# Kernel tuning notes

Hardware: AMD Instinct MI355X
Metric: run time of the kernel (lower is better)

## Reference

```python
import jax, jax.numpy as jnp
import numpy as np

HEADS = 10
DIM_HEAD = 64
C = 640
N_TOK = 1024          # (1024//32)**2 tokens per image
IMG_NUMS = 3          # total_length = id_length + 1
ID_LENGTH = 2
SA = 0.5
NEG_INF = -1e9


def _build_story_mask(key):
    # Faithful to cal_attn_mask_xl: one random row of columns shared by all
    # images, columns beyond the id_length reference images zeroed, and each
    # image's own block forced True; then broadcast over query tokens.
    L = IMG_NUMS * N_TOK
    base = jax.random.uniform(key, (1, L)) < SA                  # [1, L]
    bm = jnp.tile(base, (IMG_NUMS, 1))                           # [img, L]
    col = jnp.arange(L)
    bm = jnp.where(col[None, :] >= ID_LENGTH * N_TOK, False, bm)
    self_block = (col // N_TOK)[None, :] == jnp.arange(IMG_NUMS)[:, None]
    bm = bm | self_block                                         # [img, L]
    return jnp.repeat(bm, N_TOK, axis=0)                         # [L, L]


def setup_inputs() -> dict:
    key = jax.random.key(0)
    ks = jax.random.split(key, 7)
    B_total = 2 * IMG_NUMS
    hidden_states = jax.random.normal(ks[0], (B_total, N_TOK, C), dtype=jnp.float32)
    mask = _build_story_mask(ks[1])
    s = 1.0 / np.sqrt(C)
    Wq = jax.random.normal(ks[2], (C, HEADS * DIM_HEAD), dtype=jnp.float32) * s
    Wk = jax.random.normal(ks[3], (C, HEADS * DIM_HEAD), dtype=jnp.float32) * s
    Wv = jax.random.normal(ks[4], (C, HEADS * DIM_HEAD), dtype=jnp.float32) * s
    Wout = jax.random.normal(ks[5], (HEADS * DIM_HEAD, C), dtype=jnp.float32) * s
    bout = jnp.zeros((C,), dtype=jnp.float32)
    return {"hidden_states": hidden_states, "mask": mask,
            "Wq": Wq, "Wk": Wk, "Wv": Wv, "Wout": Wout, "bout": bout}


def reference(hidden_states, mask, Wq, Wk, Wv, Wout, bout):
    # __call1__ with encoder_hidden_states=None: fuse img_nums images into one
    # long sequence per CFG branch, then masked SDPA.
    B_total, n_tok, c = hidden_states.shape
    img_nums = B_total // 2
    L = img_nums * n_tok
    x = hidden_states.reshape(2, L, c)                       # [2, L, C]

    q = jnp.einsum('bsc,cd->bsd', x, Wq).reshape(2, L, HEADS, DIM_HEAD)
    k = jnp.einsum('bsc,cd->bsd', x, Wk).reshape(2, L, HEADS, DIM_HEAD)
    v = jnp.einsum('bsc,cd->bsd', x, Wv).reshape(2, L, HEADS, DIM_HEAD)

    scale = 1.0 / jnp.sqrt(jnp.asarray(DIM_HEAD, dtype=q.dtype))
    scores = jnp.einsum('bqhd,bkhd->bhqk', q, k) * scale     # [2, H, L, L]
    scores = jnp.where(mask[None, None, :, :], scores, NEG_INF)
    attn = jax.nn.softmax(scores, axis=-1)
    out = jnp.einsum('bhqk,bkhd->bqhd', attn, v)             # [2, L, H, Dh]
    out = out.reshape(B_total, n_tok, HEADS * DIM_HEAD)
    return jnp.einsum('bsd,dc->bsc', out, Wout) + bout
```

## Files before the change

kernel.cpp:

```cpp
#include <hip/hip_runtime.h>
#include <cstdint>
#include <cstddef>

typedef _Float16 f16;
typedef _Float16 f16x8 __attribute__((ext_vector_type(8)));
typedef _Float16 f16x4 __attribute__((ext_vector_type(4)));
typedef float f32x4 __attribute__((ext_vector_type(4)));

#define MFMA32(a, b, c) __builtin_amdgcn_mfma_f32_16x16x32_f16((a), (b), (c), 0, 0, 0)
#define MFMA16(a, b, c) __builtin_amdgcn_mfma_f32_16x16x16f16((a), (b), (c), 0, 0, 0)

#if __has_builtin(__builtin_amdgcn_exp2f)
#define EXP2F(x) __builtin_amdgcn_exp2f(x)
#else
#define EXP2F(x) exp2f(x)
#endif

#define DRAIN_MEM() __builtin_amdgcn_s_waitcnt(0x0070)

#define LOG2E 1.44269504088896340736f

__device__ __forceinline__ f16x4 pack4(float a, float b, float c, float d) {
    f16x4 r; r[0] = (f16)a; r[1] = (f16)b; r[2] = (f16)c; r[3] = (f16)d;
    return r;
}

__device__ __forceinline__ void gl_lds16(const f16* g, f16* l) {
    __builtin_amdgcn_global_load_lds((const __attribute__((address_space(1))) void*)g,
                                     (__attribute__((address_space(3))) void*)l, 16, 0, 0);
}

__global__ __launch_bounds__(256) void k_cvt_x(const float4* __restrict__ x, f16x4* __restrict__ xb) {
    const int i = blockIdx.x * 256 + threadIdx.x;
    const float4 v = x[i];
    f16x4 o;
    o[0] = (f16)v.x; o[1] = (f16)v.y; o[2] = (f16)v.z; o[3] = (f16)v.w;
    xb[i] = o;
}

__global__ __launch_bounds__(256) void k_cvt_w(const float* __restrict__ Wq, const float* __restrict__ Wk,
                                               const float* __restrict__ Wv, const float* __restrict__ Wo,
                                               f16* __restrict__ WT, f16* __restrict__ WoT) {
    __shared__ float tile[32][33];
    const int z = blockIdx.z;
    const float* src = (z == 0) ? Wq : (z == 1) ? Wk : (z == 2) ? Wv : Wo;
    f16* dst = (z < 3) ? (WT + (size_t)z * 640 * 640) : WoT;
    const float scale = (z == 0) ? 0.125f * LOG2E : 1.0f;
    const int k0 = blockIdx.x * 32, n0 = blockIdx.y * 32;
    const int t = threadIdx.x;
#pragma unroll
    for (int i = 0; i < 4; i++) {
        const int idx = i * 256 + t;
        const int r = idx >> 5, c = idx & 31;
        tile[r][c] = src[(size_t)(k0 + r) * 640 + n0 + c];
    }
    __syncthreads();
#pragma unroll
    for (int i = 0; i < 4; i++) {
        const int idx = i * 256 + t;
        const int r = idx >> 5, c = idx & 31;
        dst[(size_t)(n0 + r) * 640 + k0 + c] = (f16)(tile[c][r] * scale);
    }
}

__global__ __launch_bounds__(256) void k_gemm(const f16* __restrict__ A, const f16* __restrict__ B,
                                              f16* __restrict__ qb, f16* __restrict__ kb, f16* __restrict__ vtb) {
    __shared__ f16 As[128 * 40];
    __shared__ f16 Bs[128 * 40];
    const int t = threadIdx.x;
    const int wave = t >> 6, lane = t & 63, quad = lane >> 4, l16 = lane & 15;
    const int wm = wave >> 1, wn = wave & 1;
    const long m0 = (long)blockIdx.x * 128, n0 = (long)blockIdx.y * 128;
    const int srow = t >> 2, skc = t & 3;

    const f32x4 zero = {0.f, 0.f, 0.f, 0.f};
    f32x4 acc[4][4];
#pragma unroll
    for (int i = 0; i < 4; i++)
#pragma unroll
        for (int j = 0; j < 4; j++) acc[i][j] = zero;

    const f16* gA1 = A + (m0 + srow) * 640 + skc * 8;
    const f16* gA2 = A + (m0 + 64 + srow) * 640 + skc * 8;
    const f16* gB1 = B + (n0 + srow) * 640 + skc * 8;
    const f16* gB2 = B + (n0 + 64 + srow) * 640 + skc * 8;
    f16* sA1 = As + srow * 40 + skc * 8;
    f16* sA2 = As + (64 + srow) * 40 + skc * 8;
    f16* sB1 = Bs + srow * 40 + skc * 8;
    f16* sB2 = Bs + (64 + srow) * 40 + skc * 8;

    for (int kt = 0; kt < 20; kt++) {
        const int ko = kt * 32;
        const f16x8 a1 = *(const f16x8*)(gA1 + ko);
        const f16x8 a2 = *(const f16x8*)(gA2 + ko);
        const f16x8 b1 = *(const f16x8*)(gB1 + ko);
        const f16x8 b2 = *(const f16x8*)(gB2 + ko);
        __syncthreads();
        *(f16x8*)sA1 = a1;
        *(f16x8*)sA2 = a2;
        *(f16x8*)sB1 = b1;
        *(f16x8*)sB2 = b2;
        __syncthreads();
        f16x8 af[4], bfr[4];
#pragma unroll
        for (int mi = 0; mi < 4; mi++) af[mi] = *(const f16x8*)(As + (wm * 64 + mi * 16 + l16) * 40 + quad * 8);
#pragma unroll
        for (int ni = 0; ni < 4; ni++) bfr[ni] = *(const f16x8*)(Bs + (wn * 64 + ni * 16 + l16) * 40 + quad * 8);
#pragma unroll
        for (int mi = 0; mi < 4; mi++)
#pragma unroll
            for (int ni = 0; ni < 4; ni++) acc[mi][ni] = MFMA32(af[mi], bfr[ni], acc[mi][ni]);
    }

    const int b = (int)(m0 / 3072);
    const int which = (int)(n0 / 640);
    const int hd0 = (int)(n0 - (long)which * 640);
    if (which < 2) {
        f16* dst = (which == 0) ? qb : kb;
#pragma unroll
        for (int ni = 0; ni < 4; ni++) {
            const int hd = hd0 + wn * 64 + ni * 16 + l16;
            const int h = hd >> 6, d = hd & 63;
#pragma unroll
            for (int mi = 0; mi < 4; mi++) {
                const long l0 = m0 - (long)b * 3072 + wm * 64 + mi * 16 + quad * 4;
                f16* p = dst + ((long)(b * 10 + h) * 3072 + l0) * 64 + d;
#pragma unroll
                for (int j = 0; j < 4; j++) p[(long)j * 64] = (f16)acc[mi][ni][j];
            }
        }
    } else {
#pragma unroll
        for (int ni = 0; ni < 4; ni++) {
            const int hd = hd0 + wn * 64 + ni * 16 + l16;
            const int h = hd >> 6, d = hd & 63;
#pragma unroll
            for (int mi = 0; mi < 4; mi++) {
                const long l0 = m0 - (long)b * 3072 + wm * 64 + mi * 16 + quad * 4;
                const long col = (l0 & ~63L) + quad * 16 + mi * 4;
                f16x4 tmp;
#pragma unroll
                for (int j = 0; j < 4; j++) tmp[j] = (f16)acc[mi][ni][j];
                *(f16x4*)(vtb + ((size_t)(b * 10 + h) * 64 + d) * 3072 + col) = tmp;
            }
        }
    }
}

__global__ __launch_bounds__(256) void k_gemmo(const f16* __restrict__ A, const f16* __restrict__ B,
                                               float* __restrict__ out, const float* __restrict__ bias) {
    __shared__ f16 As[64 * 40];
    __shared__ f16 Bs[128 * 40];
    const int t = threadIdx.x;
    const int wave = t >> 6, lane = t & 63, quad = lane >> 4, l16 = lane & 15;
    const int wm = wave >> 1, wn = wave & 1;
    const long m0 = (long)blockIdx.x * 64, n0 = (long)blockIdx.y * 128;
    const int srow = t >> 2, skc = t & 3;

    const f32x4 zero = {0.f, 0.f, 0.f, 0.f};
    f32x4 acc[2][4];
#pragma unroll
    for (int i = 0; i < 2; i++)
#pragma unroll
        for (int j = 0; j < 4; j++) acc[i][j] = zero;

    const f16* gA = A + (m0 + srow) * 640 + skc * 8;
    const f16* gB1 = B + (n0 + srow) * 640 + skc * 8;
    const f16* gB2 = B + (n0 + 64 + srow) * 640 + skc * 8;
    f16* sA = As + srow * 40 + skc * 8;
    f16* sB1 = Bs + srow * 40 + skc * 8;
    f16* sB2 = Bs + (64 + srow) * 40 + skc * 8;

    for (int kt = 0; kt < 20; kt++) {
        const int ko = kt * 32;
        const f16x8 a1 = *(const f16x8*)(gA + ko);
        const f16x8 b1 = *(const f16x8*)(gB1 + ko);
        const f16x8 b2 = *(const f16x8*)(gB2 + ko);
        __syncthreads();
        *(f16x8*)sA = a1;
        *(f16x8*)sB1 = b1;
        *(f16x8*)sB2 = b2;
        __syncthreads();
        f16x8 af[2], bfr[4];
#pragma unroll
        for (int mi = 0; mi < 2; mi++) af[mi] = *(const f16x8*)(As + (wm * 32 + mi * 16 + l16) * 40 + quad * 8);
#pragma unroll
        for (int ni = 0; ni < 4; ni++) bfr[ni] = *(const f16x8*)(Bs + (wn * 64 + ni * 16 + l16) * 40 + quad * 8);
#pragma unroll
        for (int mi = 0; mi < 2; mi++)
#pragma unroll
            for (int ni = 0; ni < 4; ni++) acc[mi][ni] = MFMA32(af[mi], bfr[ni], acc[mi][ni]);
    }

#pragma unroll
    for (int ni = 0; ni < 4; ni++) {
        const long gc = n0 + wn * 64 + ni * 16 + l16;
        const float bs = bias[gc];
#pragma unroll
        for (int mi = 0; mi < 2; mi++) {
            const long r0 = m0 + wm * 32 + mi * 16 + quad * 4;
            float* p = out + r0 * 640 + gc;
#pragma unroll
            for (int j = 0; j < 4; j++) p[(long)j * 640] = acc[mi][ni][j] + bs;
        }
    }
}

__global__ __launch_bounds__(128, 2) void k_attn(const f16* __restrict__ q, const f16* __restrict__ k,
                                                 const f16* __restrict__ vT, const unsigned char* __restrict__ mask,
                                                 f16* __restrict__ ao) {
    __shared__ __align__(16) unsigned char smem[40960];

    const int t = threadIdx.x;
    const int w = t >> 6, lane = t & 63, quad = lane >> 4, l16 = lane & 15;
    const int bh = blockIdx.y, b = bh / 10, h = bh - b * 10;
    const int qt = (blockIdx.x < 16) ? (32 + (int)blockIdx.x) : ((int)blockIdx.x - 16);
    const int q0 = qt * 64;
    const int img = q0 >> 10;
    const int kmax = (img == 2) ? 3072 : 2048;
    const int nIter = kmax >> 6;
    float* bias_s = (float*)(smem + 32768);

    int mmode;
    if (mask[1] && mask[2] && mask[3]) mmode = 0;
    else if (mask[7] == 0x3f) mmode = 2;
    else mmode = 1;
    const int msz = (mmode == 0) ? 1 : 4;
    const int mhi = (mmode == 2) ? 3 : 0;
    const unsigned char* mrow = mask + (size_t)img * 1024 * 3072 * msz;

    for (int i = t; i < 2048; i += 128)
        bias_s[i] = (mrow[(size_t)i * msz + mhi] != 0) ? -8.f : -1e9f;

    const int r8 = lane >> 3, cch = lane & 7;
    const f16* kg = k + (size_t)bh * 3072 * 64;
    const f16* vg = vT + (size_t)bh * 64 * 3072;
    const int wrow0 = w * 32;

    {
        f16* K0 = (f16*)smem;
        f16* V0 = (f16*)(smem + 16384);
#pragma unroll
        for (int i = 0; i < 4; i++) {
            const int row = wrow0 + i * 8 + r8;
            gl_lds16(kg + (size_t)row * 64 + ((cch ^ (row & 7)) * 8), K0 + (wrow0 + i * 8) * 64);
            gl_lds16(vg + (size_t)row * 3072 + ((cch ^ (row & 7)) * 8), V0 + (wrow0 + i * 8) * 64);
        }
    }

    f16x8 qfA0, qfA1, qfB0, qfB1;
    {
        const f16* qp = q + ((size_t)bh * 3072 + q0 + w * 32 + l16) * 64 + quad * 8;
        qfA0 = *(const f16x8*)qp;
        qfA1 = *(const f16x8*)(qp + 32);
        qfB0 = *(const f16x8*)(qp + 16 * 64);
        qfB1 = *(const f16x8*)(qp + 16 * 64 + 32);
    }

    const int s7 = l16 & 7;
    const int bK0 = l16 * 128 + ((quad ^ s7) * 16);
    const int bK1 = l16 * 128 + (((quad + 4) ^ s7) * 16);
    const int bV0 = l16 * 128 + (((2 * quad) ^ s7) * 16);
    const int bV1 = l16 * 128 + (((2 * quad + 1) ^ s7) * 16);

    const f32x4 zero = {0.f, 0.f, 0.f, 0.f};
    f32x4 OA[4], OB[4];
#pragma unroll
    for (int i = 0; i < 4; i++) { OA[i] = zero; OB[i] = zero; }
    float lA = 0.f, lB = 0.f;

    const f32x4 m8 = {-8.f, -8.f, -8.f, -8.f};

    for (int it = 0; it < nIter; it++) {
        DRAIN_MEM();
        __syncthreads();
        const char* Kb = (const char*)smem + (it & 1) * 8192;
        const char* Vb = (const char*)smem + 16384 + (it & 1) * 8192;
        if (it + 1 < nIter) {
            const int k0n = (it + 1) << 6;
            f16* Kn = (f16*)(smem + ((it + 1) & 1) * 8192);
            f16* Vn = (f16*)(smem + 16384 + ((it + 1) & 1) * 8192);
#pragma unroll
            for (int i = 0; i < 4; i++) {
                const int row = wrow0 + i * 8 + r8;
                gl_lds16(kg + (size_t)(k0n + row) * 64 + ((cch ^ (row & 7)) * 8), Kn + (wrow0 + i * 8) * 64);
                gl_lds16(vg + (size_t)row * 3072 + k0n + ((cch ^ (row & 7)) * 8), Vn + (wrow0 + i * 8) * 64);
            }
        }

        f32x4 sA[4], sB[4];
#pragma unroll
        for (int kt = 0; kt < 4; kt++) {
            const f16x8 kf0 = *(const f16x8*)(Kb + bK0 + kt * 2048);
            const f16x8 kf1 = *(const f16x8*)(Kb + bK1 + kt * 2048);
            sA[kt] = MFMA32(kf0, qfA0, zero);
            sA[kt] = MFMA32(kf1, qfA1, sA[kt]);
            sB[kt] = MFMA32(kf0, qfB0, zero);
            sB[kt] = MFMA32(kf1, qfB1, sB[kt]);
        }
        if (it * 64 < 2048) {
#pragma unroll
            for (int kt = 0; kt < 4; kt++) {
                const f32x4 bv = *(const f32x4*)(bias_s + it * 64 + kt * 16 + quad * 4);
                sA[kt] += bv;
                sB[kt] += bv;
            }
        } else {
#pragma unroll
            for (int kt = 0; kt < 4; kt++) { sA[kt] += m8; sB[kt] += m8; }
        }

        f16x4 pkA[4], pkB[4];
#pragma unroll
        for (int kt = 0; kt < 4; kt++) {
            const float a0 = EXP2F(sA[kt][0]), a1 = EXP2F(sA[kt][1]);
            const float a2 = EXP2F(sA[kt][2]), a3 = EXP2F(sA[kt][3]);
            lA += (a0 + a1) + (a2 + a3);
            pkA[kt] = pack4(a0, a1, a2, a3);
            const float b0 = EXP2F(sB[kt][0]), b1 = EXP2F(sB[kt][1]);
            const float b2 = EXP2F(sB[kt][2]), b3 = EXP2F(sB[kt][3]);
            lB += (b0 + b1) + (b2 + b3);
            pkB[kt] = pack4(b0, b1, b2, b3);
        }

#pragma unroll
        for (int mtd = 0; mtd < 4; mtd++) {
            const f16x8 v80 = *(const f16x8*)(Vb + bV0 + mtd * 2048);
            const f16x8 v81 = *(const f16x8*)(Vb + bV1 + mtd * 2048);
            const f16x4 vf0 = __builtin_shufflevector(v80, v80, 0, 1, 2, 3);
            const f16x4 vf1 = __builtin_shufflevector(v80, v80, 4, 5, 6, 7);
            const f16x4 vf2 = __builtin_shufflevector(v81, v81, 0, 1, 2, 3);
            const f16x4 vf3 = __builtin_shufflevector(v81, v81, 4, 5, 6, 7);
            OA[mtd] = MFMA16(vf0, pkA[0], OA[mtd]);
            OA[mtd] = MFMA16(vf1, pkA[1], OA[mtd]);
            OA[mtd] = MFMA16(vf2, pkA[2], OA[mtd]);
            OA[mtd] = MFMA16(vf3, pkA[3], OA[mtd]);
            OB[mtd] = MFMA16(vf0, pkB[0], OB[mtd]);
            OB[mtd] = MFMA16(vf1, pkB[1], OB[mtd]);
            OB[mtd] = MFMA16(vf2, pkB[2], OB[mtd]);
            OB[mtd] = MFMA16(vf3, pkB[3], OB[mtd]);
        }
    }

    lA += __shfl_xor(lA, 16);
    lA += __shfl_xor(lA, 32);
    lB += __shfl_xor(lB, 16);
    lB += __shfl_xor(lB, 32);
    const float invA = 1.0f / lA;
    const float invB = 1.0f / lB;
    f16* orowA = ao + ((size_t)(b * 3072 + q0 + w * 32 + l16)) * 640 + h * 64;
    f16* orowB = orowA + (size_t)16 * 640;
#pragma unroll
    for (int mtd = 0; mtd < 4; mtd++) {
        f16x4 oa, ob;
#pragma unroll
        for (int j = 0; j < 4; j++) { oa[j] = (f16)(OA[mtd][j] * invA); ob[j] = (f16)(OB[mtd][j] * invB); }
        *(f16x4*)(orowA + mtd * 16 + quad * 4) = oa;
        *(f16x4*)(orowB + mtd * 16 + quad * 4) = ob;
    }
}

extern "C" void kernel_launch(void* const* d_in, const int* in_sizes, int n_in,
                              void* d_out, int out_size, void* d_ws, size_t ws_size,
                              hipStream_t stream) {
    (void)in_sizes; (void)n_in; (void)out_size; (void)ws_size;
    const float* x = (const float*)d_in[0];
    const unsigned char* mask = (const unsigned char*)d_in[1];
    const float* Wq = (const float*)d_in[2];
    const float* Wk = (const float*)d_in[3];
    const float* Wv = (const float*)d_in[4];
    const float* Wo = (const float*)d_in[5];
    const float* bout = (const float*)d_in[6];
    float* out = (float*)d_out;

    f16* xb  = (f16*)d_ws;
    f16* WT  = xb + 6144 * 640;
    f16* WoT = WT + 1920 * 640;
    f16* qb  = WoT + 640 * 640;
    f16* kb  = qb + 20 * 3072 * 64;
    f16* vtb = kb + 20 * 3072 * 64;

    k_cvt_x<<<3840, 256, 0, stream>>>((const float4*)x, (f16x4*)xb);
    k_cvt_w<<<dim3(20, 20, 4), 256, 0, stream>>>(Wq, Wk, Wv, Wo, WT, WoT);
    k_gemm<<<dim3(48, 15), 256, 0, stream>>>(xb, WT, qb, kb, vtb);
    k_attn<<<dim3(48, 20), 128, 0, stream>>>(qb, kb, vtb, mask, xb );
    k_gemmo<<<dim3(96, 5), 256, 0, stream>>>(xb, WoT, out, bout);
}
```

Before: 207.8 us.

## Split attention over key range with merge kernel; fuse x conversion into QKV GEMM

The attention kernel now splits each query tile's key range into two halves handled by separate blocks. Each block writes unnormalized fp32 partial outputs and row sums, and a new merge kernel adds the two halves, normalizes them and converts to fp16. This is meant to double the block count and reduce tail imbalance between images with different key lengths. The standalone fp32-to-fp16 conversion of x is removed: the QKV GEMM now reads fp32 directly and converts while loading. In exchange, the split adds fp32 partial-output traffic and one more kernel launch.

```diff
diff --git a/kernel.cpp b/kernel.cpp
--- a/kernel.cpp
+++ b/kernel.cpp
@@ -25,17 +25,16 @@
     return r;
 }
 
+__device__ __forceinline__ f16x8 cvt8(const float4 lo, const float4 hi) {
+    f16x8 r;
+    r[0] = (f16)lo.x; r[1] = (f16)lo.y; r[2] = (f16)lo.z; r[3] = (f16)lo.w;
+    r[4] = (f16)hi.x; r[5] = (f16)hi.y; r[6] = (f16)hi.z; r[7] = (f16)hi.w;
+    return r;
+}
+
 __device__ __forceinline__ void gl_lds16(const f16* g, f16* l) {
     __builtin_amdgcn_global_load_lds((const __attribute__((address_space(1))) void*)g,
                                      (__attribute__((address_space(3))) void*)l, 16, 0, 0);
-}
-
-__global__ __launch_bounds__(256) void k_cvt_x(const float4* __restrict__ x, f16x4* __restrict__ xb) {
-    const int i = blockIdx.x * 256 + threadIdx.x;
-    const float4 v = x[i];
-    f16x4 o;
-    o[0] = (f16)v.x; o[1] = (f16)v.y; o[2] = (f16)v.z; o[3] = (f16)v.w;
-    xb[i] = o;
 }
 
 __global__ __launch_bounds__(256) void k_cvt_w(const float* __restrict__ Wq, const float* __restrict__ Wk,
@@ -63,7 +62,7 @@
     }
 }
 
-__global__ __launch_bounds__(256) void k_gemm(const f16* __restrict__ A, const f16* __restrict__ B,
+__global__ __launch_bounds__(256) void k_gemm(const float* __restrict__ X, const f16* __restrict__ B,
                                               f16* __restrict__ qb, f16* __restrict__ kb, f16* __restrict__ vtb) {
     __shared__ f16 As[128 * 40];
     __shared__ f16 Bs[128 * 40];
@@ -80,8 +79,8 @@
 #pragma unroll
         for (int j = 0; j < 4; j++) acc[i][j] = zero;
 
-    const f16* gA1 = A + (m0 + srow) * 640 + skc * 8;
-    const f16* gA2 = A + (m0 + 64 + srow) * 640 + skc * 8;
+    const float* gA1 = X + (m0 + srow) * 640 + skc * 8;
+    const float* gA2 = X + (m0 + 64 + srow) * 640 + skc * 8;
     const f16* gB1 = B + (n0 + srow) * 640 + skc * 8;
     const f16* gB2 = B + (n0 + 64 + srow) * 640 + skc * 8;
     f16* sA1 = As + srow * 40 + skc * 8;
@@ -91,8 +90,8 @@
 
     for (int kt = 0; kt < 20; kt++) {
         const int ko = kt * 32;
-        const f16x8 a1 = *(const f16x8*)(gA1 + ko);
-        const f16x8 a2 = *(const f16x8*)(gA2 + ko);
+        const f16x8 a1 = cvt8(*(const float4*)(gA1 + ko), *(const float4*)(gA1 + ko + 4));
+        const f16x8 a2 = cvt8(*(const float4*)(gA2 + ko), *(const float4*)(gA2 + ko + 4));
         const f16x8 b1 = *(const f16x8*)(gB1 + ko);
         const f16x8 b2 = *(const f16x8*)(gB2 + ko);
         __syncthreads();
@@ -206,19 +205,38 @@
     }
 }
 
+__global__ __launch_bounds__(256) void k_merge(const float* __restrict__ Op, const float* __restrict__ lp,
+                                               f16* __restrict__ ao) {
+    const int i = (blockIdx.x * 256 + threadIdx.x) * 4;
+    const int qrow = i / 640;
+    const int hd = i - qrow * 640;
+    const int h = hd >> 6;
+    const float l = lp[qrow * 10 + h] + lp[61440 + qrow * 10 + h];
+    const float inv = 1.0f / l;
+    const f32x4 o0 = *(const f32x4*)(Op + i);
+    const f32x4 o1 = *(const f32x4*)(Op + (size_t)6144 * 640 + i);
+    f16x4 o;
+#pragma unroll
+    for (int j = 0; j < 4; j++) o[j] = (f16)((o0[j] + o1[j]) * inv);
+    *(f16x4*)(ao + i) = o;
+}
+
 __global__ __launch_bounds__(128, 2) void k_attn(const f16* __restrict__ q, const f16* __restrict__ k,
                                                  const f16* __restrict__ vT, const unsigned char* __restrict__ mask,
-                                                 f16* __restrict__ ao) {
+                                                 float* __restrict__ Op, float* __restrict__ lp) {
     __shared__ __align__(16) unsigned char smem[40960];
 
     const int t = threadIdx.x;
     const int w = t >> 6, lane = t & 63, quad = lane >> 4, l16 = lane & 15;
     const int bh = blockIdx.y, b = bh / 10, h = bh - b * 10;
-    const int qt = (blockIdx.x < 16) ? (32 + (int)blockIdx.x) : ((int)blockIdx.x - 16);
+    const int split = (int)blockIdx.x & 1;
+    const int qi = (int)blockIdx.x >> 1;
+    const int qt = (qi < 16) ? (32 + qi) : (qi - 16);
     const int q0 = qt * 64;
     const int img = q0 >> 10;
     const int kmax = (img == 2) ? 3072 : 2048;
-    const int nIter = kmax >> 6;
+    const int kbase = split * (kmax >> 1);
+    const int nIter = kmax >> 7;
     float* bias_s = (float*)(smem + 32768);
 
     int mmode;
@@ -243,8 +261,8 @@
 #pragma unroll
         for (int i = 0; i < 4; i++) {
             const int row = wrow0 + i * 8 + r8;
-            gl_lds16(kg + (size_t)row * 64 + ((cch ^ (row & 7)) * 8), K0 + (wrow0 + i * 8) * 64);
-            gl_lds16(vg + (size_t)row * 3072 + ((cch ^ (row & 7)) * 8), V0 + (wrow0 + i * 8) * 64);
+            gl_lds16(kg + (size_t)(kbase + row) * 64 + ((cch ^ (row & 7)) * 8), K0 + (wrow0 + i * 8) * 64);
+            gl_lds16(vg + (size_t)row * 3072 + kbase + ((cch ^ (row & 7)) * 8), V0 + (wrow0 + i * 8) * 64);
         }
     }
 
@@ -276,8 +294,9 @@
         __syncthreads();
         const char* Kb = (const char*)smem + (it & 1) * 8192;
         const char* Vb = (const char*)smem + 16384 + (it & 1) * 8192;
+        const int tb = kbase + it * 64;
         if (it + 1 < nIter) {
-            const int k0n = (it + 1) << 6;
+            const int k0n = tb + 64;
             f16* Kn = (f16*)(smem + ((it + 1) & 1) * 8192);
             f16* Vn = (f16*)(smem + 16384 + ((it + 1) & 1) * 8192);
 #pragma unroll
@@ -298,10 +317,10 @@
             sB[kt] = MFMA32(kf0, qfB0, zero);
             sB[kt] = MFMA32(kf1, qfB1, sB[kt]);
         }
-        if (it * 64 < 2048) {
+        if (tb < 2048) {
 #pragma unroll
             for (int kt = 0; kt < 4; kt++) {
-                const f32x4 bv = *(const f32x4*)(bias_s + it * 64 + kt * 16 + quad * 4);
+                const f32x4 bv = *(const f32x4*)(bias_s + tb + kt * 16 + quad * 4);
                 sA[kt] += bv;
                 sB[kt] += bv;
             }
@@ -346,17 +365,19 @@
     lA += __shfl_xor(lA, 32);
     lB += __shfl_xor(lB, 16);
     lB += __shfl_xor(lB, 32);
-    const float invA = 1.0f / lA;
-    const float invB = 1.0f / lB;
-    f16* orowA = ao + ((size_t)(b * 3072 + q0 + w * 32 + l16)) * 640 + h * 64;
-    f16* orowB = orowA + (size_t)16 * 640;
+    float* Ob = Op + (size_t)split * 6144 * 640;
+    float* lb = lp + (size_t)split * 61440;
+    const int qA = b * 3072 + q0 + w * 32 + l16;
+    if (quad == 0) {
+        lb[(size_t)qA * 10 + h] = lA;
+        lb[(size_t)(qA + 16) * 10 + h] = lB;
+    }
+    float* orowA = Ob + (size_t)qA * 640 + h * 64;
+    float* orowB = orowA + (size_t)16 * 640;
 #pragma unroll
     for (int mtd = 0; mtd < 4; mtd++) {
-        f16x4 oa, ob;
-#pragma unroll
-        for (int j = 0; j < 4; j++) { oa[j] = (f16)(OA[mtd][j] * invA); ob[j] = (f16)(OB[mtd][j] * invB); }
-        *(f16x4*)(orowA + mtd * 16 + quad * 4) = oa;
-        *(f16x4*)(orowB + mtd * 16 + quad * 4) = ob;
+        *(f32x4*)(orowA + mtd * 16 + quad * 4) = OA[mtd];
+        *(f32x4*)(orowB + mtd * 16 + quad * 4) = OB[mtd];
     }
 }
 
@@ -373,16 +394,18 @@
     const float* bout = (const float*)d_in[6];
     float* out = (float*)d_out;
 
-    f16* xb  = (f16*)d_ws;
-    f16* WT  = xb + 6144 * 640;
+    f16* WT  = (f16*)d_ws;
     f16* WoT = WT + 1920 * 640;
     f16* qb  = WoT + 640 * 640;
     f16* kb  = qb + 20 * 3072 * 64;
     f16* vtb = kb + 20 * 3072 * 64;
-
-    k_cvt_x<<<3840, 256, 0, stream>>>((const float4*)x, (f16x4*)xb);
+    f16* ao  = vtb + 20 * 3072 * 64;
+    float* Op = (float*)(ao + 6144 * 640);
+    float* lp = Op + (size_t)2 * 6144 * 640;
+
     k_cvt_w<<<dim3(20, 20, 4), 256, 0, stream>>>(Wq, Wk, Wv, Wo, WT, WoT);
-    k_gemm<<<dim3(48, 15), 256, 0, stream>>>(xb, WT, qb, kb, vtb);
-    k_attn<<<dim3(48, 20), 128, 0, stream>>>(qb, kb, vtb, mask, xb );
-    k_gemmo<<<dim3(96, 5), 256, 0, stream>>>(xb, WoT, out, bout);
-}
+    k_gemm<<<dim3(48, 15), 256, 0, stream>>>(x, WT, qb, kb, vtb);
+    k_attn<<<dim3(96, 20), 128, 0, stream>>>(qb, kb, vtb, mask, Op, lp);
+    k_merge<<<3840, 256, 0, stream>>>(Op, lp, ao);
+    k_gemmo<<<dim3(96, 5), 256, 0, stream>>>(ao, WoT, out, bout);
+}
```

After: 217.0 us. 4.4% more time.

## Fuse x conversion into QKV GEMM, precompute mask bias, single-wave attention blocks

Applied to the files above, without the earlier changes.

Drops the separate fp32-to-fp16 conversion kernel for x, so the QKV GEMM now reads fp32 activations and converts them while staging into LDS. The mask-to-bias table is built once by a small kernel into global memory, replacing the per-block LDS fill in the attention kernel. Attention blocks shrink from two waves to one, each loading full K/V tiles itself and waiting only on its own vmcnt instead of a block barrier, with twice as many blocks. In exchange the GEMM reads twice the A bytes, the bias is now read from global memory every iteration, and each wave issues twice as many async loads.

```diff
diff --git a/kernel.cpp b/kernel.cpp
--- a/kernel.cpp
+++ b/kernel.cpp
@@ -16,7 +16,7 @@
 #define EXP2F(x) exp2f(x)
 #endif
 
-#define DRAIN_MEM() __builtin_amdgcn_s_waitcnt(0x0070)
+#define WAIT_VM0() __builtin_amdgcn_s_waitcnt(0x0F70)
 
 #define LOG2E 1.44269504088896340736f
 
@@ -25,17 +25,30 @@
     return r;
 }
 
+__device__ __forceinline__ f16x8 cvt8(const float4 lo, const float4 hi) {
+    f16x8 r;
+    r[0] = (f16)lo.x; r[1] = (f16)lo.y; r[2] = (f16)lo.z; r[3] = (f16)lo.w;
+    r[4] = (f16)hi.x; r[5] = (f16)hi.y; r[6] = (f16)hi.z; r[7] = (f16)hi.w;
+    return r;
+}
+
 __device__ __forceinline__ void gl_lds16(const f16* g, f16* l) {
     __builtin_amdgcn_global_load_lds((const __attribute__((address_space(1))) void*)g,
                                      (__attribute__((address_space(3))) void*)l, 16, 0, 0);
 }
 
-__global__ __launch_bounds__(256) void k_cvt_x(const float4* __restrict__ x, f16x4* __restrict__ xb) {
+__global__ __launch_bounds__(256) void k_bias(const unsigned char* __restrict__ mask,
+                                              float* __restrict__ bias_g) {
+    int mmode;
+    if (mask[1] && mask[2] && mask[3]) mmode = 0;
+    else if (mask[7] == 0x3f) mmode = 2;
+    else mmode = 1;
+    const int msz = (mmode == 0) ? 1 : 4;
+    const int mhi = (mmode == 2) ? 3 : 0;
     const int i = blockIdx.x * 256 + threadIdx.x;
-    const float4 v = x[i];
-    f16x4 o;
-    o[0] = (f16)v.x; o[1] = (f16)v.y; o[2] = (f16)v.z; o[3] = (f16)v.w;
-    xb[i] = o;
+    const int img = i / 3072, c = i - img * 3072;
+    const unsigned char* mrow = mask + (size_t)img * 1024 * 3072 * msz;
+    bias_g[i] = (mrow[(size_t)c * msz + mhi] != 0) ? -8.f : -1e9f;
 }
 
 __global__ __launch_bounds__(256) void k_cvt_w(const float* __restrict__ Wq, const float* __restrict__ Wk,
@@ -63,7 +76,7 @@
     }
 }
 
-__global__ __launch_bounds__(256) void k_gemm(const f16* __restrict__ A, const f16* __restrict__ B,
+__global__ __launch_bounds__(256) void k_gemm(const float* __restrict__ X, const f16* __restrict__ B,
                                               f16* __restrict__ qb, f16* __restrict__ kb, f16* __restrict__ vtb) {
     __shared__ f16 As[128 * 40];
     __shared__ f16 Bs[128 * 40];
@@ -80,8 +93,8 @@
 #pragma unroll
         for (int j = 0; j < 4; j++) acc[i][j] = zero;
 
-    const f16* gA1 = A + (m0 + srow) * 640 + skc * 8;
-    const f16* gA2 = A + (m0 + 64 + srow) * 640 + skc * 8;
+    const float* gA1 = X + (m0 + srow) * 640 + skc * 8;
+    const float* gA2 = X + (m0 + 64 + srow) * 640 + skc * 8;
     const f16* gB1 = B + (n0 + srow) * 640 + skc * 8;
     const f16* gB2 = B + (n0 + 64 + srow) * 640 + skc * 8;
     f16* sA1 = As + srow * 40 + skc * 8;
@@ -91,8 +104,8 @@
 
     for (int kt = 0; kt < 20; kt++) {
         const int ko = kt * 32;
-        const f16x8 a1 = *(const f16x8*)(gA1 + ko);
-        const f16x8 a2 = *(const f16x8*)(gA2 + ko);
+        const f16x8 a1 = cvt8(*(const float4*)(gA1 + ko), *(const float4*)(gA1 + ko + 4));
+        const f16x8 a2 = cvt8(*(const float4*)(gA2 + ko), *(const float4*)(gA2 + ko + 4));
         const f16x8 b1 = *(const f16x8*)(gB1 + ko);
         const f16x8 b2 = *(const f16x8*)(gB2 + ko);
         __syncthreads();
@@ -206,51 +219,39 @@
     }
 }
 
-__global__ __launch_bounds__(128, 2) void k_attn(const f16* __restrict__ q, const f16* __restrict__ k,
-                                                 const f16* __restrict__ vT, const unsigned char* __restrict__ mask,
-                                                 f16* __restrict__ ao) {
-    __shared__ __align__(16) unsigned char smem[40960];
-
-    const int t = threadIdx.x;
-    const int w = t >> 6, lane = t & 63, quad = lane >> 4, l16 = lane & 15;
+__global__ __launch_bounds__(64, 2) void k_attn(const f16* __restrict__ q, const f16* __restrict__ k,
+                                                const f16* __restrict__ vT, const float* __restrict__ bias_g,
+                                                f16* __restrict__ ao) {
+    __shared__ __align__(16) unsigned char smem[32768];
+
+    const int lane = threadIdx.x;
+    const int quad = lane >> 4, l16 = lane & 15;
     const int bh = blockIdx.y, b = bh / 10, h = bh - b * 10;
-    const int qt = (blockIdx.x < 16) ? (32 + (int)blockIdx.x) : ((int)blockIdx.x - 16);
-    const int q0 = qt * 64;
+    const int wt = (blockIdx.x < 32) ? (64 + (int)blockIdx.x) : ((int)blockIdx.x - 32);
+    const int q0 = wt * 32;
     const int img = q0 >> 10;
     const int kmax = (img == 2) ? 3072 : 2048;
     const int nIter = kmax >> 6;
-    float* bias_s = (float*)(smem + 32768);
-
-    int mmode;
-    if (mask[1] && mask[2] && mask[3]) mmode = 0;
-    else if (mask[7] == 0x3f) mmode = 2;
-    else mmode = 1;
-    const int msz = (mmode == 0) ? 1 : 4;
-    const int mhi = (mmode == 2) ? 3 : 0;
-    const unsigned char* mrow = mask + (size_t)img * 1024 * 3072 * msz;
-
-    for (int i = t; i < 2048; i += 128)
-        bias_s[i] = (mrow[(size_t)i * msz + mhi] != 0) ? -8.f : -1e9f;
+    const float* bg = bias_g + img * 3072;
 
     const int r8 = lane >> 3, cch = lane & 7;
     const f16* kg = k + (size_t)bh * 3072 * 64;
     const f16* vg = vT + (size_t)bh * 64 * 3072;
-    const int wrow0 = w * 32;
 
     {
         f16* K0 = (f16*)smem;
         f16* V0 = (f16*)(smem + 16384);
 #pragma unroll
-        for (int i = 0; i < 4; i++) {
-            const int row = wrow0 + i * 8 + r8;
-            gl_lds16(kg + (size_t)row * 64 + ((cch ^ (row & 7)) * 8), K0 + (wrow0 + i * 8) * 64);
-            gl_lds16(vg + (size_t)row * 3072 + ((cch ^ (row & 7)) * 8), V0 + (wrow0 + i * 8) * 64);
+        for (int i = 0; i < 8; i++) {
+            const int row = i * 8 + r8;
+            gl_lds16(kg + (size_t)row * 64 + ((cch ^ (row & 7)) * 8), K0 + i * 8 * 64);
+            gl_lds16(vg + (size_t)row * 3072 + ((cch ^ (row & 7)) * 8), V0 + i * 8 * 64);
         }
     }
 
     f16x8 qfA0, qfA1, qfB0, qfB1;
     {
-        const f16* qp = q + ((size_t)bh * 3072 + q0 + w * 32 + l16) * 64 + quad * 8;
+        const f16* qp = q + ((size_t)bh * 3072 + q0 + l16) * 64 + quad * 8;
         qfA0 = *(const f16x8*)qp;
         qfA1 = *(const f16x8*)(qp + 32);
         qfB0 = *(const f16x8*)(qp + 16 * 64);
@@ -269,24 +270,26 @@
     for (int i = 0; i < 4; i++) { OA[i] = zero; OB[i] = zero; }
     float lA = 0.f, lB = 0.f;
 
-    const f32x4 m8 = {-8.f, -8.f, -8.f, -8.f};
-
     for (int it = 0; it < nIter; it++) {
-        DRAIN_MEM();
-        __syncthreads();
+        WAIT_VM0();
         const char* Kb = (const char*)smem + (it & 1) * 8192;
         const char* Vb = (const char*)smem + 16384 + (it & 1) * 8192;
+        const int tb = it * 64;
         if (it + 1 < nIter) {
-            const int k0n = (it + 1) << 6;
+            const int k0n = tb + 64;
             f16* Kn = (f16*)(smem + ((it + 1) & 1) * 8192);
             f16* Vn = (f16*)(smem + 16384 + ((it + 1) & 1) * 8192);
 #pragma unroll
-            for (int i = 0; i < 4; i++) {
-                const int row = wrow0 + i * 8 + r8;
-                gl_lds16(kg + (size_t)(k0n + row) * 64 + ((cch ^ (row & 7)) * 8), Kn + (wrow0 + i * 8) * 64);
-                gl_lds16(vg + (size_t)row * 3072 + k0n + ((cch ^ (row & 7)) * 8), Vn + (wrow0 + i * 8) * 64);
+            for (int i = 0; i < 8; i++) {
+                const int row = i * 8 + r8;
+                gl_lds16(kg + (size_t)(k0n + row) * 64 + ((cch ^ (row & 7)) * 8), Kn + i * 8 * 64);
+                gl_lds16(vg + (size_t)row * 3072 + k0n + ((cch ^ (row & 7)) * 8), Vn + i * 8 * 64);
             }
         }
+
+        f32x4 bv[4];
+#pragma unroll
+        for (int kt = 0; kt < 4; kt++) bv[kt] = *(const f32x4*)(bg + tb + kt * 16 + quad * 4);
 
         f32x4 sA[4], sB[4];
 #pragma unroll
@@ -298,17 +301,8 @@
             sB[kt] = MFMA32(kf0, qfB0, zero);
             sB[kt] = MFMA32(kf1, qfB1, sB[kt]);
         }
-        if (it * 64 < 2048) {
-#pragma unroll
-            for (int kt = 0; kt < 4; kt++) {
-                const f32x4 bv = *(const f32x4*)(bias_s + it * 64 + kt * 16 + quad * 4);
-                sA[kt] += bv;
-                sB[kt] += bv;
-            }
-        } else {
-#pragma unroll
-            for (int kt = 0; kt < 4; kt++) { sA[kt] += m8; sB[kt] += m8; }
-        }
+#pragma unroll
+        for (int kt = 0; kt < 4; kt++) { sA[kt] += bv[kt]; sB[kt] += bv[kt]; }
 
         f16x4 pkA[4], pkB[4];
 #pragma unroll
@@ -348,7 +342,7 @@
     lB += __shfl_xor(lB, 32);
     const float invA = 1.0f / lA;
     const float invB = 1.0f / lB;
-    f16* orowA = ao + ((size_t)(b * 3072 + q0 + w * 32 + l16)) * 640 + h * 64;
+    f16* orowA = ao + ((size_t)(b * 3072 + q0 + l16)) * 640 + h * 64;
     f16* orowB = orowA + (size_t)16 * 640;
 #pragma unroll
     for (int mtd = 0; mtd < 4; mtd++) {
@@ -373,16 +367,17 @@
     const float* bout = (const float*)d_in[6];
     float* out = (float*)d_out;
 
-    f16* xb  = (f16*)d_ws;
-    f16* WT  = xb + 6144 * 640;
+    f16* WT  = (f16*)d_ws;
     f16* WoT = WT + 1920 * 640;
     f16* qb  = WoT + 640 * 640;
     f16* kb  = qb + 20 * 3072 * 64;
     f16* vtb = kb + 20 * 3072 * 64;
-
-    k_cvt_x<<<3840, 256, 0, stream>>>((const float4*)x, (f16x4*)xb);
+    f16* ao  = vtb + 20 * 3072 * 64;
+    float* bias_g = (float*)(ao + 6144 * 640);
+
     k_cvt_w<<<dim3(20, 20, 4), 256, 0, stream>>>(Wq, Wk, Wv, Wo, WT, WoT);
-    k_gemm<<<dim3(48, 15), 256, 0, stream>>>(xb, WT, qb, kb, vtb);
-    k_attn<<<dim3(48, 20), 128, 0, stream>>>(qb, kb, vtb, mask, xb );
-    k_gemmo<<<dim3(96, 5), 256, 0, stream>>>(xb, WoT, out, bout);
-}
+    k_bias<<<36, 256, 0, stream>>>(mask, bias_g);
+    k_gemm<<<dim3(48, 15), 256, 0, stream>>>(x, WT, qb, kb, vtb);
+    k_attn<<<dim3(96, 20), 64, 0, stream>>>(qb, kb, vtb, bias_g, ao);
+    k_gemmo<<<dim3(96, 5), 256, 0, stream>>>(ao, WoT, out, bout);
+}
```

New measurement: 275.4 us. +32.5%, slower.

## Double attention query tile per block and merge conversion kernels into one launch

Applied to the files above, without the earlier changes.

The attention kernel now gives each wave 64 query rows (four 16-row chunks) instead of 32, so each K/V tile staged in LDS is reused across twice as many queries and the grid shrinks from 48 to 24 blocks per head. Score computation, bias add, exp and packing are fused into one loop per key subtile. The x and weight conversion kernels are merged into a single launch, and the attention output goes to a separate workspace buffer rather than overwriting xb. In exchange, register pressure rises sharply (16 output accumulators per wave) and there are fewer blocks for 256 CUs, which may hurt occupancy and load balance.

```diff
diff --git a/kernel.cpp b/kernel.cpp
--- a/kernel.cpp
+++ b/kernel.cpp
@@ -30,24 +30,28 @@
                                      (__attribute__((address_space(3))) void*)l, 16, 0, 0);
 }
 
-__global__ __launch_bounds__(256) void k_cvt_x(const float4* __restrict__ x, f16x4* __restrict__ xb) {
-    const int i = blockIdx.x * 256 + threadIdx.x;
-    const float4 v = x[i];
-    f16x4 o;
-    o[0] = (f16)v.x; o[1] = (f16)v.y; o[2] = (f16)v.z; o[3] = (f16)v.w;
-    xb[i] = o;
-}
-
-__global__ __launch_bounds__(256) void k_cvt_w(const float* __restrict__ Wq, const float* __restrict__ Wk,
-                                               const float* __restrict__ Wv, const float* __restrict__ Wo,
-                                               f16* __restrict__ WT, f16* __restrict__ WoT) {
+__global__ __launch_bounds__(256) void k_prep(const float4* __restrict__ x4, f16x4* __restrict__ xb,
+                                              const float* __restrict__ Wq, const float* __restrict__ Wk,
+                                              const float* __restrict__ Wv, const float* __restrict__ Wo,
+                                              f16* __restrict__ WT, f16* __restrict__ WoT) {
     __shared__ float tile[32][33];
-    const int z = blockIdx.z;
+    const int t = threadIdx.x;
+    if (blockIdx.x < 3840) {
+        const int i = blockIdx.x * 256 + t;
+        const float4 v = x4[i];
+        f16x4 o;
+        o[0] = (f16)v.x; o[1] = (f16)v.y; o[2] = (f16)v.z; o[3] = (f16)v.w;
+        xb[i] = o;
+        return;
+    }
+    const int bi = blockIdx.x - 3840;
+    const int z = bi / 400;
+    const int rem = bi - z * 400;
+    const int bx = rem / 20, by = rem - (rem / 20) * 20;
     const float* src = (z == 0) ? Wq : (z == 1) ? Wk : (z == 2) ? Wv : Wo;
     f16* dst = (z < 3) ? (WT + (size_t)z * 640 * 640) : WoT;
     const float scale = (z == 0) ? 0.125f * LOG2E : 1.0f;
-    const int k0 = blockIdx.x * 32, n0 = blockIdx.y * 32;
-    const int t = threadIdx.x;
+    const int k0 = bx * 32, n0 = by * 32;
 #pragma unroll
     for (int i = 0; i < 4; i++) {
         const int idx = i * 256 + t;
@@ -214,8 +218,8 @@
     const int t = threadIdx.x;
     const int w = t >> 6, lane = t & 63, quad = lane >> 4, l16 = lane & 15;
     const int bh = blockIdx.y, b = bh / 10, h = bh - b * 10;
-    const int qt = (blockIdx.x < 16) ? (32 + (int)blockIdx.x) : ((int)blockIdx.x - 16);
-    const int q0 = qt * 64;
+    const int qt = (blockIdx.x < 8) ? (16 + (int)blockIdx.x) : ((int)blockIdx.x - 8);
+    const int q0 = qt * 128;
     const int img = q0 >> 10;
     const int kmax = (img == 2) ? 3072 : 2048;
     const int nIter = kmax >> 6;
@@ -248,13 +252,12 @@
         }
     }
 
-    f16x8 qfA0, qfA1, qfB0, qfB1;
-    {
-        const f16* qp = q + ((size_t)bh * 3072 + q0 + w * 32 + l16) * 64 + quad * 8;
-        qfA0 = *(const f16x8*)qp;
-        qfA1 = *(const f16x8*)(qp + 32);
-        qfB0 = *(const f16x8*)(qp + 16 * 64);
-        qfB1 = *(const f16x8*)(qp + 16 * 64 + 32);
+    f16x8 qf[4][2];
+#pragma unroll
+    for (int c = 0; c < 4; c++) {
+        const f16* qp = q + ((size_t)bh * 3072 + q0 + w * 64 + c * 16 + l16) * 64 + quad * 8;
+        qf[c][0] = *(const f16x8*)qp;
+        qf[c][1] = *(const f16x8*)(qp + 32);
     }
 
     const int s7 = l16 & 7;
@@ -264,10 +267,12 @@
     const int bV1 = l16 * 128 + (((2 * quad + 1) ^ s7) * 16);
 
     const f32x4 zero = {0.f, 0.f, 0.f, 0.f};
-    f32x4 OA[4], OB[4];
-#pragma unroll
-    for (int i = 0; i < 4; i++) { OA[i] = zero; OB[i] = zero; }
-    float lA = 0.f, lB = 0.f;
+    f32x4 O[4][4];
+#pragma unroll
+    for (int c = 0; c < 4; c++)
+#pragma unroll
+        for (int m = 0; m < 4; m++) O[c][m] = zero;
+    float l_i[4] = {0.f, 0.f, 0.f, 0.f};
 
     const f32x4 m8 = {-8.f, -8.f, -8.f, -8.f};
 
@@ -276,8 +281,9 @@
         __syncthreads();
         const char* Kb = (const char*)smem + (it & 1) * 8192;
         const char* Vb = (const char*)smem + 16384 + (it & 1) * 8192;
+        const int tb = it * 64;
         if (it + 1 < nIter) {
-            const int k0n = (it + 1) << 6;
+            const int k0n = tb + 64;
             f16* Kn = (f16*)(smem + ((it + 1) & 1) * 8192);
             f16* Vn = (f16*)(smem + 16384 + ((it + 1) & 1) * 8192);
 #pragma unroll
@@ -288,39 +294,23 @@
             }
         }
 
-        f32x4 sA[4], sB[4];
+        f16x4 pk[4][4];
 #pragma unroll
         for (int kt = 0; kt < 4; kt++) {
             const f16x8 kf0 = *(const f16x8*)(Kb + bK0 + kt * 2048);
             const f16x8 kf1 = *(const f16x8*)(Kb + bK1 + kt * 2048);
-            sA[kt] = MFMA32(kf0, qfA0, zero);
-            sA[kt] = MFMA32(kf1, qfA1, sA[kt]);
-            sB[kt] = MFMA32(kf0, qfB0, zero);
-            sB[kt] = MFMA32(kf1, qfB1, sB[kt]);
-        }
-        if (it * 64 < 2048) {
-#pragma unroll
-            for (int kt = 0; kt < 4; kt++) {
-                const f32x4 bv = *(const f32x4*)(bias_s + it * 64 + kt * 16 + quad * 4);
-                sA[kt] += bv;
-                sB[kt] += bv;
-            }
-        } else {
-#pragma unroll
-            for (int kt = 0; kt < 4; kt++) { sA[kt] += m8; sB[kt] += m8; }
-        }
-
-        f16x4 pkA[4], pkB[4];
-#pragma unroll
-        for (int kt = 0; kt < 4; kt++) {
-            const float a0 = EXP2F(sA[kt][0]), a1 = EXP2F(sA[kt][1]);
-            const float a2 = EXP2F(sA[kt][2]), a3 = EXP2F(sA[kt][3]);
-            lA += (a0 + a1) + (a2 + a3);
-            pkA[kt] = pack4(a0, a1, a2, a3);
-            const float b0 = EXP2F(sB[kt][0]), b1 = EXP2F(sB[kt][1]);
-            const float b2 = EXP2F(sB[kt][2]), b3 = EXP2F(sB[kt][3]);
-            lB += (b0 + b1) + (b2 + b3);
-            pkB[kt] = pack4(b0, b1, b2, b3);
+            f32x4 bv = m8;
+            if (tb < 2048) bv = *(const f32x4*)(bias_s + tb + kt * 16 + quad * 4);
+#pragma unroll
+            for (int c = 0; c < 4; c++) {
+                f32x4 s = MFMA32(kf0, qf[c][0], zero);
+                s = MFMA32(kf1, qf[c][1], s);
+                s += bv;
+                const float p0 = EXP2F(s[0]), p1 = EXP2F(s[1]);
+                const float p2 = EXP2F(s[2]), p3 = EXP2F(s[3]);
+                l_i[c] += (p0 + p1) + (p2 + p3);
+                pk[c][kt] = pack4(p0, p1, p2, p3);
+            }
         }
 
 #pragma unroll
@@ -331,32 +321,29 @@
             const f16x4 vf1 = __builtin_shufflevector(v80, v80, 4, 5, 6, 7);
             const f16x4 vf2 = __builtin_shufflevector(v81, v81, 0, 1, 2, 3);
             const f16x4 vf3 = __builtin_shufflevector(v81, v81, 4, 5, 6, 7);
-            OA[mtd] = MFMA16(vf0, pkA[0], OA[mtd]);
-            OA[mtd] = MFMA16(vf1, pkA[1], OA[mtd]);
-            OA[mtd] = MFMA16(vf2, pkA[2], OA[mtd]);
-            OA[mtd] = MFMA16(vf3, pkA[3], OA[mtd]);
-            OB[mtd] = MFMA16(vf0, pkB[0], OB[mtd]);
-            OB[mtd] = MFMA16(vf1, pkB[1], OB[mtd]);
-            OB[mtd] = MFMA16(vf2, pkB[2], OB[mtd]);
-            OB[mtd] = MFMA16(vf3, pkB[3], OB[mtd]);
-        }
-    }
-
-    lA += __shfl_xor(lA, 16);
-    lA += __shfl_xor(lA, 32);
-    lB += __shfl_xor(lB, 16);
-    lB += __shfl_xor(lB, 32);
-    const float invA = 1.0f / lA;
-    const float invB = 1.0f / lB;
-    f16* orowA = ao + ((size_t)(b * 3072 + q0 + w * 32 + l16)) * 640 + h * 64;
-    f16* orowB = orowA + (size_t)16 * 640;
-#pragma unroll
-    for (int mtd = 0; mtd < 4; mtd++) {
-        f16x4 oa, ob;
-#pragma unroll
-        for (int j = 0; j < 4; j++) { oa[j] = (f16)(OA[mtd][j] * invA); ob[j] = (f16)(OB[mtd][j] * invB); }
-        *(f16x4*)(orowA + mtd * 16 + quad * 4) = oa;
-        *(f16x4*)(orowB + mtd * 16 + quad * 4) = ob;
+#pragma unroll
+            for (int c = 0; c < 4; c++) {
+                O[c][mtd] = MFMA16(vf0, pk[c][0], O[c][mtd]);
+                O[c][mtd] = MFMA16(vf1, pk[c][1], O[c][mtd]);
+                O[c][mtd] = MFMA16(vf2, pk[c][2], O[c][mtd]);
+                O[c][mtd] = MFMA16(vf3, pk[c][3], O[c][mtd]);
+            }
+        }
+    }
+
+#pragma unroll
+    for (int c = 0; c < 4; c++) {
+        l_i[c] += __shfl_xor(l_i[c], 16);
+        l_i[c] += __shfl_xor(l_i[c], 32);
+        const float inv = 1.0f / l_i[c];
+        f16* orow = ao + ((size_t)(b * 3072 + q0 + w * 64 + c * 16 + l16)) * 640 + h * 64;
+#pragma unroll
+        for (int mtd = 0; mtd < 4; mtd++) {
+            f16x4 o;
+#pragma unroll
+            for (int j = 0; j < 4; j++) o[j] = (f16)(O[c][mtd][j] * inv);
+            *(f16x4*)(orow + mtd * 16 + quad * 4) = o;
+        }
     }
 }
 
@@ -379,10 +366,10 @@
     f16* qb  = WoT + 640 * 640;
     f16* kb  = qb + 20 * 3072 * 64;
     f16* vtb = kb + 20 * 3072 * 64;
-
-    k_cvt_x<<<3840, 256, 0, stream>>>((const float4*)x, (f16x4*)xb);
-    k_cvt_w<<<dim3(20, 20, 4), 256, 0, stream>>>(Wq, Wk, Wv, Wo, WT, WoT);
+    f16* ao  = vtb + 20 * 3072 * 64;
+
+    k_prep<<<5440, 256, 0, stream>>>((const float4*)x, (f16x4*)xb, Wq, Wk, Wv, Wo, WT, WoT);
     k_gemm<<<dim3(48, 15), 256, 0, stream>>>(xb, WT, qb, kb, vtb);
-    k_attn<<<dim3(48, 20), 128, 0, stream>>>(qb, kb, vtb, mask, xb );
-    k_gemmo<<<dim3(96, 5), 256, 0, stream>>>(xb, WoT, out, bout);
-}
+    k_attn<<<dim3(24, 20), 128, 0, stream>>>(qb, kb, vtb, mask, ao);
+    k_gemmo<<<dim3(96, 5), 256, 0, stream>>>(ao, WoT, out, bout);
+}
```

Result: slower. 237.5 us (+14.3%).
